# Kernel tuning notes

Hardware: AMD Instinct MI355X
Metric: run time of the kernel (lower is better)

## Reference

```python
import jax, jax.numpy as jnp
import numpy as np

B, N, D, H = 1, 4096, 768, 12
HD = D // H
SCALE = HD ** -0.5

def setup_inputs() -> dict:
    key = jax.random.key(0)
    k1, k2, k3 = jax.random.split(key, 3)
    x = jax.random.normal(k1, (B, N, D), dtype=jnp.float32)
    W_qkv = jax.random.normal(k2, (D, 3 * D), dtype=jnp.float32) * (D ** -0.5)
    W_out = jax.random.normal(k3, (D, D), dtype=jnp.float32) * (D ** -0.5)
    b_out = jnp.zeros((D,), dtype=jnp.float32)
    return {"x": x, "W_qkv": W_qkv, "W_out": W_out, "b_out": b_out}

def reference(x, W_qkv, W_out, b_out):
    # qkv projection: (B,N,3D)
    qkv = x @ W_qkv
    q, k, v = jnp.split(qkv, 3, axis=-1)
    # (B,N,D) -> (B,H,N,hd)
    def heads(t):
        return t.reshape(B, N, H, HD).transpose(0, 2, 1, 3)
    q, k, v = heads(q), heads(k), heads(v)
    scores = jnp.einsum('bhnd,bhmd->bhnm', q, k) * SCALE  # (B,H,N,N)
    attn = jax.nn.softmax(scores, axis=-1)
    out = jnp.einsum('bhnm,bhmd->bhnd', attn, v)
    out = out.transpose(0, 2, 1, 3).reshape(B, N, D)
    return out @ W_out + b_out
```

## Files before the change

kernel.cpp:

```cpp
#include <hip/hip_runtime.h>
#include <hip/hip_bf16.h>
#include <math.h>

typedef __attribute__((ext_vector_type(8))) short bf16x8;
typedef __attribute__((ext_vector_type(4))) short bf16x4;
typedef __attribute__((ext_vector_type(4))) float floatx4;

constexpr int kN  = 4096;
constexpr int kD  = 768;
constexpr int kH  = 12;
constexpr int kHD = 64;
constexpr int k3D = 2304;
constexpr float kQScale = 0.18033688011112042f;

static __device__ __forceinline__ short f2b(float f) {
    __hip_bfloat16 h = __float2bfloat16(f);
    return *reinterpret_cast<short*>(&h);
}

static __device__ __forceinline__ float fast_exp2(float x) {
#if __has_builtin(__builtin_amdgcn_exp2f)
    return __builtin_amdgcn_exp2f(x);
#else
    return exp2f(x);
#endif
}

static __device__ __forceinline__ void async_copy16(const void* g, void* l) {
    __builtin_amdgcn_global_load_lds(
        (const __attribute__((address_space(1))) void*)g,
        (__attribute__((address_space(3))) void*)l, 16, 0, 0);
}

constexpr int kBlkX  = 1536;
constexpr int kBlkWq = 72 * 24;
constexpr int kBlkWo = 24 * 24;

__global__ __launch_bounds__(256)
void prep(const float* __restrict__ x, const float* __restrict__ Wq,
          const float* __restrict__ Wo, short* __restrict__ Xb,
          short* __restrict__ WqT, short* __restrict__ WoT)
{
    const int bid = blockIdx.x;
    const int tid = threadIdx.x;
    if (bid < kBlkX) {
        const int i = bid * 256 + tid;
        const float4* s = reinterpret_cast<const float4*>(x + (size_t)i * 8);
        float4 a = s[0], b = s[1];
        bf16x8 v;
        v[0] = f2b(a.x); v[1] = f2b(a.y); v[2] = f2b(a.z); v[3] = f2b(a.w);
        v[4] = f2b(b.x); v[5] = f2b(b.y); v[6] = f2b(b.z); v[7] = f2b(b.w);
        *reinterpret_cast<bf16x8*>(Xb + (size_t)i * 8) = v;
        return;
    }
    const float* src; short* dst; int R, C, bx, by;
    if (bid < kBlkX + kBlkWq) {
        const int local = bid - kBlkX;
        src = Wq; dst = WqT; R = kD; C = k3D; bx = local % 72; by = local / 72;
    } else {
        const int local = bid - kBlkX - kBlkWq;
        src = Wo; dst = WoT; R = kD; C = kD; bx = local % 24; by = local / 24;
    }
    __shared__ float t[32][33];
    const int c0 = bx * 32, r0 = by * 32;
    const int tx = tid & 31, ty = tid >> 5;
    #pragma unroll
    for (int i = ty; i < 32; i += 8)
        t[i][tx] = src[(size_t)(r0 + i) * C + c0 + tx];
    __syncthreads();
    #pragma unroll
    for (int i = ty; i < 32; i += 8)
        dst[(size_t)(c0 + i) * R + r0 + tx] = f2b(t[tx][i]);
}

template<int MODE>
__device__ __forceinline__
void gemm_core(const short* __restrict__ A, const short* __restrict__ BT,
               const float* __restrict__ bias, float* __restrict__ Cout,
               short* __restrict__ Qh, short* __restrict__ Kh, short* __restrict__ Vt,
               int N, int K)
{
    const int bm   = blockIdx.x * 128;
    const int bn   = blockIdx.y * 128;
    const int tid  = threadIdx.x;
    const int wave = tid >> 6;
    const int lane = tid & 63;
    const int l15  = lane & 15;
    const int quad = lane >> 4;
    const int l3   = l15 & 3;

    __shared__ alignas(16) short As[128 * 32];
    __shared__ alignas(16) short Bs[128 * 32];

    floatx4 acc[4][4] = {};
    const int wm = (wave >> 1) * 64;
    const int wn = (wave & 1) * 64;

    const int srl = lane >> 2;
    const int scc = (lane & 3) ^ (srl & 3);

    for (int k0 = 0; k0 < K; k0 += 32) {
        __syncthreads();
        #pragma unroll
        for (int j = 0; j < 2; ++j) {
            const int rs = 32 * wave + 16 * j;
            async_copy16(&A [(size_t)(bm + rs + srl) * K + k0 + 8 * scc], &As[rs * 32]);
            async_copy16(&BT[(size_t)(bn + rs + srl) * K + k0 + 8 * scc], &Bs[rs * 32]);
        }
        __syncthreads();

        bf16x8 af[4], bfr[4];
        #pragma unroll
        for (int mt = 0; mt < 4; ++mt)
            af[mt] = *reinterpret_cast<const bf16x8*>(&As[(wm + 16 * mt + l15) * 32 + 8 * (quad ^ l3)]);
        #pragma unroll
        for (int nt = 0; nt < 4; ++nt)
            bfr[nt] = *reinterpret_cast<const bf16x8*>(&Bs[(wn + 16 * nt + l15) * 32 + 8 * (quad ^ l3)]);
        #pragma unroll
        for (int mt = 0; mt < 4; ++mt)
            #pragma unroll
            for (int nt = 0; nt < 4; ++nt)
                acc[mt][nt] = __builtin_amdgcn_mfma_f32_16x16x32_bf16(af[mt], bfr[nt], acc[mt][nt], 0, 0, 0);
    }

    #pragma unroll
    for (int mt = 0; mt < 4; ++mt) {
        #pragma unroll
        for (int nt = 0; nt < 4; ++nt) {
            #pragma unroll
            for (int r = 0; r < 4; ++r) {
                const int row = bm + wm + mt * 16 + 4 * quad + r;
                const int col = bn + wn + nt * 16 + l15;
                float v = acc[mt][nt][r];
                if (MODE == 0) {
                    Cout[(size_t)row * N + col] = v + bias[col];
                } else {
                    const int proj   = col / kD;
                    const int within = col - proj * kD;
                    const int h = within >> 6;
                    const int d = within & 63;
                    if (proj == 0)      Qh[((size_t)h * kN + row) * kHD + d] = f2b(v * kQScale);
                    else if (proj == 1) Kh[((size_t)h * kN + row) * kHD + d] = f2b(v);
                    else                Vt[((size_t)h * kHD + d) * kN + row] = f2b(v);
                }
            }
        }
    }
}

__global__ __launch_bounds__(256)
void gemm_qkv(const short* __restrict__ A, const short* __restrict__ BT,
              short* __restrict__ Qh, short* __restrict__ Kh, short* __restrict__ Vt)
{
    gemm_core<1>(A, BT, nullptr, nullptr, Qh, Kh, Vt, k3D, kD);
}

__global__ __launch_bounds__(256)
void gemm_out(const short* __restrict__ A, const short* __restrict__ BT,
              const float* __restrict__ bias, float* __restrict__ Cout)
{
    gemm_core<0>(A, BT, bias, Cout, nullptr, nullptr, nullptr, kD, kD);
}

__global__ __launch_bounds__(128)
void attn(const short* __restrict__ Qh, const short* __restrict__ Kh,
          const short* __restrict__ Vt, short* __restrict__ AO)
{
    const int flat = blockIdx.y * 64 + blockIdx.x;
    const int W    = (flat & 7) * 96 + (flat >> 3);
    const int h    = W >> 6;
    const int q0   = (W & 63) * 64;

    const int tid  = threadIdx.x;
    const int wave = tid >> 6;
    const int lane = tid & 63;
    const int l15  = lane & 15;
    const int quad = lane >> 4;
    const int lx   = l15 & 7;

    __shared__ alignas(16) short Ks[2][64 * 64];
    __shared__ alignas(16) short Vs[2][64 * 64];
    __shared__ alignas(16) short Pm[2][32 * 64];

    bf16x8 qf[2][2];
    {
        const size_t qb = ((size_t)h * kN + q0 + 32 * wave + l15) * kHD;
        #pragma unroll
        for (int mt = 0; mt < 2; ++mt)
            #pragma unroll
            for (int s = 0; s < 2; ++s)
                qf[mt][s] = *reinterpret_cast<const bf16x8*>(
                    &Qh[qb + (size_t)(16 * mt) * kHD + 32 * s + 8 * quad]);
    }

    bf16x8 onesf;
    #pragma unroll
    for (int i = 0; i < 8; ++i) onesf[i] = (short)0x3F80;

    floatx4 oacc[2][4] = {};
    floatx4 dacc[2] = {};

    const int srl = lane >> 3;
    const int scc = (lane & 7) ^ srl;

    short* Pw = Pm[wave];

    const size_t kbase = (size_t)h * kN * kHD;
    const size_t vbase = (size_t)h * kHD * kN;

    auto stage = [&](int b, int kv0) {
        #pragma unroll
        for (int j = 0; j < 4; ++j) {
            const int r0 = 32 * wave + 8 * j;
            async_copy16(&Kh[kbase + (size_t)(kv0 + r0 + srl) * kHD + 8 * scc],
                         &Ks[b][r0 * 64]);
            async_copy16(&Vt[vbase + (size_t)(r0 + srl) * kN + kv0 + 8 * scc],
                         &Vs[b][r0 * 64]);
        }
    };

    constexpr int kNT = kN / 64;
    int cur = 0;
    stage(0, 0);

    for (int t = 0; t < kNT; ++t) {
        __syncthreads();
        if (t + 1 < kNT) stage(cur ^ 1, (t + 1) * 64);

        const short* Kc = Ks[cur];
        const short* Vc = Vs[cur];

        #pragma unroll
        for (int nt = 0; nt < 4; ++nt) {
            bf16x8 kf0 = *reinterpret_cast<const bf16x8*>(
                &Kc[(16 * nt + l15) * 64 + 8 * ((quad) ^ lx)]);
            bf16x8 kf1 = *reinterpret_cast<const bf16x8*>(
                &Kc[(16 * nt + l15) * 64 + 8 * ((4 + quad) ^ lx)]);
            floatx4 sacc[2] = {};
            __builtin_amdgcn_s_setprio(1);
            #pragma unroll
            for (int mt = 0; mt < 2; ++mt) {
                sacc[mt] = __builtin_amdgcn_mfma_f32_16x16x32_bf16(kf0, qf[mt][0], sacc[mt], 0, 0, 0);
                sacc[mt] = __builtin_amdgcn_mfma_f32_16x16x32_bf16(kf1, qf[mt][1], sacc[mt], 0, 0, 0);
            }
            __builtin_amdgcn_s_setprio(0);
            #pragma unroll
            for (int mt = 0; mt < 2; ++mt) {
                const float p0 = fast_exp2(sacc[mt][0]);
                const float p1 = fast_exp2(sacc[mt][1]);
                const float p2 = fast_exp2(sacc[mt][2]);
                const float p3 = fast_exp2(sacc[mt][3]);
                bf16x4 pk;
                pk[0] = f2b(p0); pk[1] = f2b(p1); pk[2] = f2b(p2); pk[3] = f2b(p3);
                const int c = 2 * nt + (quad >> 1);
                *reinterpret_cast<bf16x4*>(
                    &Pw[mt * 1024 + l15 * 64 + 8 * (c ^ lx) + 4 * (quad & 1)]) = pk;
            }
        }

        __builtin_amdgcn_s_setprio(1);
        #pragma unroll
        for (int s = 0; s < 2; ++s) {
            bf16x8 vv[4];
            #pragma unroll
            for (int dt = 0; dt < 4; ++dt)
                vv[dt] = *reinterpret_cast<const bf16x8*>(
                    &Vc[(16 * dt + l15) * 64 + 8 * ((4 * s + quad) ^ lx)]);
            #pragma unroll
            for (int mt = 0; mt < 2; ++mt) {
                bf16x8 pa = *reinterpret_cast<const bf16x8*>(
                    &Pw[mt * 1024 + l15 * 64 + 8 * ((4 * s + quad) ^ lx)]);
                dacc[mt] = __builtin_amdgcn_mfma_f32_16x16x32_bf16(pa, onesf, dacc[mt], 0, 0, 0);
                #pragma unroll
                for (int dt = 0; dt < 4; ++dt)
                    oacc[mt][dt] = __builtin_amdgcn_mfma_f32_16x16x32_bf16(
                        pa, vv[dt], oacc[mt][dt], 0, 0, 0);
            }
        }
        __builtin_amdgcn_s_setprio(0);

        cur ^= 1;
    }

    #pragma unroll
    for (int mt = 0; mt < 2; ++mt) {
        float inv[4];
        #pragma unroll
        for (int r = 0; r < 4; ++r) inv[r] = 1.0f / dacc[mt][r];
        #pragma unroll
        for (int dt = 0; dt < 4; ++dt) {
            #pragma unroll
            for (int r = 0; r < 4; ++r) {
                const int row = q0 + 32 * wave + 16 * mt + 4 * quad + r;
                const int col = h * kHD + 16 * dt + l15;
                AO[(size_t)row * kD + col] = f2b(oacc[mt][dt][r] * inv[r]);
            }
        }
    }
}

extern "C" void kernel_launch(void* const* d_in, const int* in_sizes, int n_in,
                              void* d_out, int out_size, void* d_ws, size_t ws_size,
                              hipStream_t stream)
{
    const float* x     = (const float*)d_in[0];
    const float* W_qkv = (const float*)d_in[1];
    const float* W_out = (const float*)d_in[2];
    const float* b_out = (const float*)d_in[3];
    float* out = (float*)d_out;

    const size_t HNHD = (size_t)kH * kN * kHD;
    short* Qh    = (short*)d_ws;
    short* Kh    = Qh + HNHD;
    short* Vt    = Kh + HNHD;
    short* Xb    = Vt + HNHD;
    short* WqkvT = Xb + (size_t)kN * kD;
    short* WoutT = WqkvT + (size_t)k3D * kD;
    short* AO    = Xb;
    (void)in_sizes; (void)n_in; (void)out_size; (void)ws_size;

    prep<<<dim3(kBlkX + kBlkWq + kBlkWo), dim3(256), 0, stream>>>(
        x, W_qkv, W_out, Xb, WqkvT, WoutT);

    gemm_qkv<<<dim3(kN / 128, k3D / 128), dim3(256), 0, stream>>>(
        Xb, WqkvT, Qh, Kh, Vt);
    attn<<<dim3(kN / 64, kH), dim3(128), 0, stream>>>(Qh, Kh, Vt, AO);
    gemm_out<<<dim3(kN / 128, kD / 128), dim3(256), 0, stream>>>(
        AO, WoutT, b_out, out);
}
```

Baseline: 217.6 us.

## Split attention KV tile across wave pairs and keep P in registers via permlane

The attention block grows from two to four waves. Each pair of waves splits every 64-key tile in half (32 keys each), and the two partial output and denominator accumulators are reduced through shared memory at the end. The probability tile is no longer round-tripped through LDS. Its fragments are packed with v_cvt_pk_bf16 and rearranged with permlane32/16 swaps to form the A operand of the PV MFMA directly. This is meant to raise wave-level parallelism and cut LDS traffic, at the cost of a final cross-wave reduction and reliance on gfx950-specific instructions.

```diff
diff --git a/kernel.cpp b/kernel.cpp
--- a/kernel.cpp
+++ b/kernel.cpp
@@ -5,6 +5,7 @@
 typedef __attribute__((ext_vector_type(8))) short bf16x8;
 typedef __attribute__((ext_vector_type(4))) short bf16x4;
 typedef __attribute__((ext_vector_type(4))) float floatx4;
+typedef __attribute__((ext_vector_type(4))) unsigned int uint4v;
 
 constexpr int kN  = 4096;
 constexpr int kD  = 768;
@@ -24,6 +25,18 @@
 #else
     return exp2f(x);
 #endif
+}
+
+static __device__ __forceinline__ unsigned cvt_pk_bf16(float lo, float hi) {
+    unsigned r;
+    asm("v_cvt_pk_bf16_f32 %0, %1, %2" : "=v"(r) : "v"(lo), "v"(hi));
+    return r;
+}
+static __device__ __forceinline__ void permlane32_swap(unsigned &a, unsigned &b) {
+    asm("v_permlane32_swap_b32 %0, %1" : "+v"(a), "+v"(b));
+}
+static __device__ __forceinline__ void permlane16_swap(unsigned &a, unsigned &b) {
+    asm("v_permlane16_swap_b32 %0, %1" : "+v"(a), "+v"(b));
 }
 
 static __device__ __forceinline__ void async_copy16(const void* g, void* l) {
@@ -162,7 +175,7 @@
     gemm_core<0>(A, BT, bias, Cout, nullptr, nullptr, nullptr, kD, kD);
 }
 
-__global__ __launch_bounds__(128)
+__global__ __launch_bounds__(256)
 void attn(const short* __restrict__ Qh, const short* __restrict__ Kh,
           const short* __restrict__ Vt, short* __restrict__ AO)
 {
@@ -177,14 +190,17 @@
     const int l15  = lane & 15;
     const int quad = lane >> 4;
     const int lx   = l15 & 7;
-
-    __shared__ alignas(16) short Ks[2][64 * 64];
-    __shared__ alignas(16) short Vs[2][64 * 64];
-    __shared__ alignas(16) short Pm[2][32 * 64];
+    const int wm   = wave >> 1;
+    const int wk   = wave & 1;
+
+    __shared__ alignas(16) short smem[16384];
+    __shared__ float Dr[2][2][16];
+    short* Ks0 = smem;
+    short* Vs0 = smem + 8192;
 
     bf16x8 qf[2][2];
     {
-        const size_t qb = ((size_t)h * kN + q0 + 32 * wave + l15) * kHD;
+        const size_t qb = ((size_t)h * kN + q0 + 32 * wm + l15) * kHD;
         #pragma unroll
         for (int mt = 0; mt < 2; ++mt)
             #pragma unroll
@@ -203,19 +219,17 @@
     const int srl = lane >> 3;
     const int scc = (lane & 7) ^ srl;
 
-    short* Pw = Pm[wave];
-
     const size_t kbase = (size_t)h * kN * kHD;
     const size_t vbase = (size_t)h * kHD * kN;
 
     auto stage = [&](int b, int kv0) {
         #pragma unroll
-        for (int j = 0; j < 4; ++j) {
-            const int r0 = 32 * wave + 8 * j;
+        for (int j = 0; j < 2; ++j) {
+            const int r0 = 16 * wave + 8 * j;
             async_copy16(&Kh[kbase + (size_t)(kv0 + r0 + srl) * kHD + 8 * scc],
-                         &Ks[b][r0 * 64]);
+                         Ks0 + b * 4096 + r0 * 64);
             async_copy16(&Vt[vbase + (size_t)(r0 + srl) * kN + kv0 + 8 * scc],
-                         &Vs[b][r0 * 64]);
+                         Vs0 + b * 4096 + r0 * 64);
         }
     };
 
@@ -227,73 +241,104 @@
         __syncthreads();
         if (t + 1 < kNT) stage(cur ^ 1, (t + 1) * 64);
 
-        const short* Kc = Ks[cur];
-        const short* Vc = Vs[cur];
-
-        #pragma unroll
-        for (int nt = 0; nt < 4; ++nt) {
-            bf16x8 kf0 = *reinterpret_cast<const bf16x8*>(
-                &Kc[(16 * nt + l15) * 64 + 8 * ((quad) ^ lx)]);
-            bf16x8 kf1 = *reinterpret_cast<const bf16x8*>(
-                &Kc[(16 * nt + l15) * 64 + 8 * ((4 + quad) ^ lx)]);
-            floatx4 sacc[2] = {};
-            __builtin_amdgcn_s_setprio(1);
-            #pragma unroll
-            for (int mt = 0; mt < 2; ++mt) {
-                sacc[mt] = __builtin_amdgcn_mfma_f32_16x16x32_bf16(kf0, qf[mt][0], sacc[mt], 0, 0, 0);
-                sacc[mt] = __builtin_amdgcn_mfma_f32_16x16x32_bf16(kf1, qf[mt][1], sacc[mt], 0, 0, 0);
+        const short* Kc = Ks0 + cur * 4096;
+        const short* Vc = Vs0 + cur * 4096;
+
+        floatx4 sacc[2][2] = {};
+        __builtin_amdgcn_s_setprio(1);
+        #pragma unroll
+        for (int nt = 0; nt < 2; ++nt) {
+            #pragma unroll
+            for (int s = 0; s < 2; ++s) {
+                bf16x8 kf = *reinterpret_cast<const bf16x8*>(
+                    &Kc[(32 * wk + 16 * nt + l15) * 64 + 8 * ((4 * s + quad) ^ lx)]);
+                #pragma unroll
+                for (int mt = 0; mt < 2; ++mt)
+                    sacc[mt][nt] = __builtin_amdgcn_mfma_f32_16x16x32_bf16(
+                        kf, qf[mt][s], sacc[mt][nt], 0, 0, 0);
             }
-            __builtin_amdgcn_s_setprio(0);
-            #pragma unroll
-            for (int mt = 0; mt < 2; ++mt) {
-                const float p0 = fast_exp2(sacc[mt][0]);
-                const float p1 = fast_exp2(sacc[mt][1]);
-                const float p2 = fast_exp2(sacc[mt][2]);
-                const float p3 = fast_exp2(sacc[mt][3]);
-                bf16x4 pk;
-                pk[0] = f2b(p0); pk[1] = f2b(p1); pk[2] = f2b(p2); pk[3] = f2b(p3);
-                const int c = 2 * nt + (quad >> 1);
-                *reinterpret_cast<bf16x4*>(
-                    &Pw[mt * 1024 + l15 * 64 + 8 * (c ^ lx) + 4 * (quad & 1)]) = pk;
-            }
+        }
+        __builtin_amdgcn_s_setprio(0);
+
+        bf16x8 pa[2];
+        #pragma unroll
+        for (int mt = 0; mt < 2; ++mt) {
+            float e[2][4];
+            #pragma unroll
+            for (int nt = 0; nt < 2; ++nt)
+                #pragma unroll
+                for (int r = 0; r < 4; ++r)
+                    e[nt][r] = fast_exp2(sacc[mt][nt][r]);
+            unsigned x0 = cvt_pk_bf16(e[0][0], e[0][1]);
+            unsigned y0 = cvt_pk_bf16(e[1][0], e[1][1]);
+            unsigned x1 = cvt_pk_bf16(e[0][2], e[0][3]);
+            unsigned y1 = cvt_pk_bf16(e[1][2], e[1][3]);
+            permlane32_swap(x0, y0);
+            permlane16_swap(x0, y0);
+            permlane32_swap(x1, y1);
+            permlane16_swap(x1, y1);
+            union { uint4v u; bf16x8 v; } pu;
+            pu.u[0] = x0; pu.u[1] = x1; pu.u[2] = y0; pu.u[3] = y1;
+            pa[mt] = pu.v;
         }
 
         __builtin_amdgcn_s_setprio(1);
         #pragma unroll
-        for (int s = 0; s < 2; ++s) {
-            bf16x8 vv[4];
+        for (int dt = 0; dt < 4; ++dt) {
+            bf16x8 vv = *reinterpret_cast<const bf16x8*>(
+                &Vc[(16 * dt + l15) * 64 + 8 * ((4 * wk + quad) ^ lx)]);
+            #pragma unroll
+            for (int mt = 0; mt < 2; ++mt)
+                oacc[mt][dt] = __builtin_amdgcn_mfma_f32_16x16x32_bf16(
+                    pa[mt], vv, oacc[mt][dt], 0, 0, 0);
+        }
+        #pragma unroll
+        for (int mt = 0; mt < 2; ++mt)
+            dacc[mt] = __builtin_amdgcn_mfma_f32_16x16x32_bf16(
+                pa[mt], onesf, dacc[mt], 0, 0, 0);
+        __builtin_amdgcn_s_setprio(0);
+
+        cur ^= 1;
+    }
+
+    __syncthreads();
+    float* red = reinterpret_cast<float*>(smem);
+    if (wk == 1) {
+        #pragma unroll
+        for (int mt = 0; mt < 2; ++mt)
             #pragma unroll
             for (int dt = 0; dt < 4; ++dt)
-                vv[dt] = *reinterpret_cast<const bf16x8*>(
-                    &Vc[(16 * dt + l15) * 64 + 8 * ((4 * s + quad) ^ lx)]);
-            #pragma unroll
-            for (int mt = 0; mt < 2; ++mt) {
-                bf16x8 pa = *reinterpret_cast<const bf16x8*>(
-                    &Pw[mt * 1024 + l15 * 64 + 8 * ((4 * s + quad) ^ lx)]);
-                dacc[mt] = __builtin_amdgcn_mfma_f32_16x16x32_bf16(pa, onesf, dacc[mt], 0, 0, 0);
+                *reinterpret_cast<floatx4*>(
+                    &red[wm * 2048 + (mt * 4 + dt) * 256 + l15 * 16 + quad * 4]) =
+                    oacc[mt][dt];
+        if (l15 == 0) {
+            #pragma unroll
+            for (int mt = 0; mt < 2; ++mt)
                 #pragma unroll
-                for (int dt = 0; dt < 4; ++dt)
-                    oacc[mt][dt] = __builtin_amdgcn_mfma_f32_16x16x32_bf16(
-                        pa, vv[dt], oacc[mt][dt], 0, 0, 0);
-            }
-        }
-        __builtin_amdgcn_s_setprio(0);
-
-        cur ^= 1;
-    }
-
-    #pragma unroll
-    for (int mt = 0; mt < 2; ++mt) {
-        float inv[4];
-        #pragma unroll
-        for (int r = 0; r < 4; ++r) inv[r] = 1.0f / dacc[mt][r];
-        #pragma unroll
-        for (int dt = 0; dt < 4; ++dt) {
-            #pragma unroll
-            for (int r = 0; r < 4; ++r) {
-                const int row = q0 + 32 * wave + 16 * mt + 4 * quad + r;
-                const int col = h * kHD + 16 * dt + l15;
-                AO[(size_t)row * kD + col] = f2b(oacc[mt][dt][r] * inv[r]);
+                for (int r = 0; r < 4; ++r)
+                    Dr[wm][mt][4 * quad + r] = dacc[mt][r];
+        }
+    }
+    __syncthreads();
+    if (wk == 0) {
+        #pragma unroll
+        for (int mt = 0; mt < 2; ++mt) {
+            #pragma unroll
+            for (int dt = 0; dt < 4; ++dt)
+                oacc[mt][dt] += *reinterpret_cast<const floatx4*>(
+                    &red[wm * 2048 + (mt * 4 + dt) * 256 + l15 * 16 + quad * 4]);
+            float inv[4];
+            #pragma unroll
+            for (int r = 0; r < 4; ++r)
+                inv[r] = 1.0f / (dacc[mt][r] + Dr[wm][mt][4 * quad + r]);
+            #pragma unroll
+            for (int dt = 0; dt < 4; ++dt) {
+                #pragma unroll
+                for (int r = 0; r < 4; ++r) {
+                    const int row = q0 + 32 * wm + 16 * mt + 4 * quad + r;
+                    const int col = h * kHD + 16 * dt + l15;
+                    AO[(size_t)row * kD + col] = f2b(oacc[mt][dt][r] * inv[r]);
+                }
             }
         }
     }
@@ -324,7 +369,7 @@
 
     gemm_qkv<<<dim3(kN / 128, k3D / 128), dim3(256), 0, stream>>>(
         Xb, WqkvT, Qh, Kh, Vt);
-    attn<<<dim3(kN / 64, kH), dim3(128), 0, stream>>>(Qh, Kh, Vt, AO);
+    attn<<<dim3(kN / 64, kH), dim3(256), 0, stream>>>(Qh, Kh, Vt, AO);
     gemm_out<<<dim3(kN / 128, kD / 128), dim3(256), 0, stream>>>(
         AO, WoutT, b_out, out);
 }
```

Measured after the change: 212.3 us. -2.4%, faster.
